# Kernel tuning notes

Measured on AMD Instinct MI355X. Metric: run time of the kernel, lower is better.

## Reference

```python
import jax, jax.numpy as jnp
import numpy as np

BS, T, D, H = 1024, 8, 512, 512  # batch, seq_length, input_dim, hidden_dim


def setup_inputs() -> dict:
    key = jax.random.key(0)
    ks = jax.random.split(key, 9)
    s = lambda k, shape, sc=1.0: jax.random.normal(k, shape, dtype=jnp.float32) * sc
    return {
        "x": s(ks[0], (BS, T, D)),
        "h0": s(ks[1], (2, 1, H)),
        "c0": s(ks[2], (2, 1, H)),
        # per-direction LSTM params; b = b_ih + b_hh combined (identical math)
        "W_ih_f": s(ks[3], (4 * H, D), 0.05),
        "W_hh_f": s(ks[4], (4 * H, H), 0.05),
        "b_f": s(ks[5], (4 * H,), 0.05),
        "W_ih_b": s(ks[6], (4 * H, D), 0.05),
        "W_hh_b": s(ks[7], (4 * H, H), 0.05),
        "b_b": s(ks[8], (4 * H,), 0.05),
    }


def _dir_scan(xg, h0, c0, W_hh):
    """One LSTM direction as a single continuous scan.
    xg: (N, 4H) precomputed input-gate contributions (x @ W_ih.T + b)
    h0, c0: (H,) initial state; W_hh: (4H, H).
    """
    Wt = W_hh.T  # (H, 4H)

    def step(carry, g):
        h, c = carry
        z = g + h @ Wt  # (4H,)
        i, f, gg, o = jnp.split(z, 4)  # PyTorch gate order: i, f, g, o
        i = jax.nn.sigmoid(i)
        f = jax.nn.sigmoid(f)
        gg = jnp.tanh(gg)
        o = jax.nn.sigmoid(o)
        c = f * c + i * gg
        h = o * jnp.tanh(c)
        return (h, c), h

    (hN, cN), hs = jax.lax.scan(step, (h0, c0), xg)
    return hs, hN, cN


def reference(x, h0, c0, W_ih_f, W_hh_f, b_f, W_ih_b, W_hh_b, b_b):
    bs, t, d = x.shape
    hdim = W_hh_f.shape[1]
    # Hidden state is threaded across batch elements in the original loop, so:
    # forward dir == one scan over the flattened (bs*T) sequence,
    # backward dir == one scan over per-sample-reversed then flattened sequence.
    xf = x.reshape(bs * t, d)
    xb = x[:, ::-1, :].reshape(bs * t, d)
    gf = xf @ W_ih_f.T + b_f  # (bs*T, 4H)
    gb = xb @ W_ih_b.T + b_b
    hs_f, hNf, cNf = _dir_scan(gf, h0[0, 0], c0[0, 0], W_hh_f)
    hs_b, hNb, cNb = _dir_scan(gb, h0[1, 0], c0[1, 0], W_hh_b)
    hs_f = hs_f.reshape(bs, t, hdim)
    hs_b = hs_b.reshape(bs, t, hdim)[:, ::-1, :]  # undo per-sample reversal
    out = jnp.concatenate([hs_f, hs_b], axis=-1).reshape(bs * t, 2 * hdim)
    h_n = jnp.stack([hNf, hNb])[:, None, :]  # (2, 1, H)
    c_n = jnp.stack([cNf, cNb])[:, None, :]
    return out, h_n, c_n
```

## Files before the change

kernel.cpp:

```cpp
#include <hip/hip_runtime.h>
#include <stdint.h>

#define BSZ   1024
#define TT    8
#define DD    512
#define HH    512
#define NSEQ  (BSZ*TT)
#define FOURH (4*HH)
#define POISON 0xAAAAAAAAu
#define G_ELEMS  ((size_t)2*NSEQ*FOURH)
#define HB_ELEMS ((size_t)2*(NSEQ+1)*HH)
#define POLL_CAP (1<<16)

typedef __attribute__((ext_vector_type(4))) float vf4;

__device__ __forceinline__ void ld2x16_ic(const float* p, vf4& a, vf4& b){
  asm volatile("global_load_dwordx4 %0, %2, off sc0 sc1\n\t"
               "global_load_dwordx4 %1, %2, off offset:16 sc0 sc1\n\t"
               "s_waitcnt vmcnt(0)"
               : "=v"(a), "=v"(b) : "v"(p) : "memory");
}
__device__ __forceinline__ void st_ic(float* p, float v){
  asm volatile("global_store_dword %0, %1, off sc0 sc1"
               :: "v"(p), "v"(v) : "memory");
}

__global__ void init_hbuf_k(float* __restrict__ hbuf, const float* __restrict__ h0)
{
  size_t idx = (size_t)blockIdx.x*blockDim.x + threadIdx.x;
  if (idx >= HB_ELEMS) return;
  int j = (int)(idx % HH);
  size_t r = idx / HH;
  int t   = (int)(r % (NSEQ+1));
  int dir = (int)(r / (NSEQ+1));
  uint32_t v;
  if (t == 0){
    uint32_t u = __float_as_uint(h0[dir*HH + j]);
    if (u == POISON) u ^= 1u;
    v = u;
  } else {
    v = POISON;
  }
  ((uint32_t*)hbuf)[idx] = v;
}

__global__ __launch_bounds__(256) void gemm_ih_k(
    const float* __restrict__ x,
    const float* __restrict__ Wf, const float* __restrict__ bf,
    const float* __restrict__ Wb, const float* __restrict__ bb,
    float* __restrict__ g)
{
  const int bm = blockIdx.x;
  const int bn = blockIdx.y;
  const int n0  = bm*64;
  const int m0g = bn*64;
  const int dir = m0g >> 11;
  const int m0  = m0g & 2047;
  const float* __restrict__ W    = dir ? Wb : Wf;
  const float* __restrict__ bias = dir ? bb : bf;

  __shared__ float As[32][68];
  __shared__ float Bs[32][68];

  const int tid = threadIdx.x;
  const int tx = tid & 15, ty = tid >> 4;
  float acc[4][4] = {};

  const int lr = tid >> 2;
  const int lk = (tid & 3) * 8;
  int arow = n0 + lr; if (dir) arow ^= 7;
  const float* ap = &x[(size_t)arow*DD];
  const float* wp = &W[(size_t)(m0+lr)*DD];

  for (int k0 = 0; k0 < DD; k0 += 32){
    float4 a0 = *(const float4*)&ap[k0+lk];
    float4 a1 = *(const float4*)&ap[k0+lk+4];
    float4 w0 = *(const float4*)&wp[k0+lk];
    float4 w1 = *(const float4*)&wp[k0+lk+4];
    __syncthreads();
    As[lk+0][lr]=a0.x; As[lk+1][lr]=a0.y; As[lk+2][lr]=a0.z; As[lk+3][lr]=a0.w;
    As[lk+4][lr]=a1.x; As[lk+5][lr]=a1.y; As[lk+6][lr]=a1.z; As[lk+7][lr]=a1.w;
    Bs[lk+0][lr]=w0.x; Bs[lk+1][lr]=w0.y; Bs[lk+2][lr]=w0.z; Bs[lk+3][lr]=w0.w;
    Bs[lk+4][lr]=w1.x; Bs[lk+5][lr]=w1.y; Bs[lk+6][lr]=w1.z; Bs[lk+7][lr]=w1.w;
    __syncthreads();
    #pragma unroll
    for (int kk = 0; kk < 32; kk++){
      float4 av = *(const float4*)&As[kk][ty*4];
      float4 bv = *(const float4*)&Bs[kk][tx*4];
      acc[0][0]+=av.x*bv.x; acc[0][1]+=av.x*bv.y; acc[0][2]+=av.x*bv.z; acc[0][3]+=av.x*bv.w;
      acc[1][0]+=av.y*bv.x; acc[1][1]+=av.y*bv.y; acc[1][2]+=av.y*bv.z; acc[1][3]+=av.y*bv.w;
      acc[2][0]+=av.z*bv.x; acc[2][1]+=av.z*bv.y; acc[2][2]+=av.z*bv.z; acc[2][3]+=av.z*bv.w;
      acc[3][0]+=av.w*bv.x; acc[3][1]+=av.w*bv.y; acc[3][2]+=av.w*bv.z; acc[3][3]+=av.w*bv.w;
    }
  }

  const size_t gbase = (size_t)dir*NSEQ*FOURH;
  #pragma unroll
  for (int i = 0; i < 4; i++){
    const int n = n0 + ty*4 + i;
    #pragma unroll
    for (int j = 0; j < 4; j++){
      const int m = m0 + tx*4 + j;
      g[gbase + (size_t)n*FOURH + m] = acc[i][j] + bias[m];
    }
  }
}

#define DPP_ROR_ADD(v, ctrl) do { \
    int _t = __builtin_amdgcn_update_dpp(0, __float_as_int(v), (ctrl), 0xf, 0xf, false); \
    (v) += __int_as_float(_t); } while (0)

__global__ __launch_bounds__(1024, 4) void scan_k(
    const float* __restrict__ Whh_f, const float* __restrict__ Whh_b,
    const float* __restrict__ c0, const float* __restrict__ g,
    float* __restrict__ hbuf, float* __restrict__ out)
{
  const int bx  = blockIdx.x;
  const int dir = bx >> 5;
  const int w   = bx & 31;
  const int j0  = w << 4;
  const int tid  = threadIdx.x;
  const int lane = tid & 63;
  const int wv   = tid >> 6;
  const int s    = lane & 31;
  const int rb   = lane >> 5;
  const int r0   = (wv << 2) + rb;
  const int r1   = r0 + 2;

  const float* __restrict__ Whh = dir ? Whh_b : Whh_f;

  __shared__ vf4  hsh4[128];
  __shared__ float zbuf[64];
  __shared__ float gsh[64];
  __shared__ int dead;

  float wA[16], wB[16];
  {
    const int gA = r0 >> 4, hA = r0 & 15;
    const int gB = r1 >> 4, hB = r1 & 15;
    const float* pa = &Whh[(size_t)(gA*HH + j0 + hA)*HH + (s<<4)];
    const float* pb = &Whh[(size_t)(gB*HH + j0 + hB)*HH + (s<<4)];
    #pragma unroll
    for (int q = 0; q < 4; q++){
      float4 va = ((const float4*)pa)[q];
      wA[4*q+0]=va.x; wA[4*q+1]=va.y; wA[4*q+2]=va.z; wA[4*q+3]=va.w;
      float4 vb = ((const float4*)pb)[q];
      wB[4*q+0]=vb.x; wB[4*q+1]=vb.y; wB[4*q+2]=vb.z; wB[4*q+3]=vb.w;
    }
  }

  float cst = 0.f;
  if (tid < 16) cst = c0[dir*HH + j0 + tid];
  if (tid == 0) dead = 0;
  __syncthreads();

  float* __restrict__ hb = hbuf + (size_t)dir*(NSEQ+1)*HH;
  const float* __restrict__ gbp = g + (size_t)dir*NSEQ*FOURH;

  const bool gloader = (tid >= 64) && (tid < 80);
  const int  gl = tid - 64;

  for (int t = 0; t < NSEQ; t++){
    float pgi=0.f, pgf=0.f, pgg=0.f, pgo=0.f;
    if (gloader){
      const float* gp = &gbp[(size_t)t*FOURH + j0 + gl];
      pgi = gp[0]; pgf = gp[HH]; pgg = gp[2*HH]; pgo = gp[3*HH];
    }

    if (wv == 0){
      const float* hp = &hb[(size_t)t*HH + (lane<<3)];
      vf4 a, b;
      int it = 0;
      for (;;){
        ld2x16_ic(hp, a, b);
        bool ok = (__float_as_uint(a.x)!=POISON) & (__float_as_uint(a.y)!=POISON)
                & (__float_as_uint(a.z)!=POISON) & (__float_as_uint(a.w)!=POISON)
                & (__float_as_uint(b.x)!=POISON) & (__float_as_uint(b.y)!=POISON)
                & (__float_as_uint(b.z)!=POISON) & (__float_as_uint(b.w)!=POISON);
        if (ok) break;
        if (++it > POLL_CAP){ dead = 1; break; }
        __builtin_amdgcn_s_sleep(1);
      }
      const int c0i = lane << 1;
      const int xo  = (c0i >> 3) & 3;
      hsh4[c0i ^ xo]       = a;
      hsh4[(c0i + 1) ^ xo] = b;
    }
    __syncthreads();
    if (dead) break;

    vf4 h4a, h4b, h4c, h4d;
    {
      const int cb = s << 2;
      h4a = hsh4[(cb+0) ^ (((cb+0)>>3)&3)];
      h4b = hsh4[(cb+1) ^ (((cb+1)>>3)&3)];
      h4c = hsh4[(cb+2) ^ (((cb+2)>>3)&3)];
      h4d = hsh4[(cb+3) ^ (((cb+3)>>3)&3)];
    }

    float a0=0.f, a1=0.f, b0=0.f, b1=0.f;
    a0 += wA[ 0]*h4a.x; a1 += wA[ 1]*h4a.y; a0 += wA[ 2]*h4a.z; a1 += wA[ 3]*h4a.w;
    a0 += wA[ 4]*h4b.x; a1 += wA[ 5]*h4b.y; a0 += wA[ 6]*h4b.z; a1 += wA[ 7]*h4b.w;
    a0 += wA[ 8]*h4c.x; a1 += wA[ 9]*h4c.y; a0 += wA[10]*h4c.z; a1 += wA[11]*h4c.w;
    a0 += wA[12]*h4d.x; a1 += wA[13]*h4d.y; a0 += wA[14]*h4d.z; a1 += wA[15]*h4d.w;
    b0 += wB[ 0]*h4a.x; b1 += wB[ 1]*h4a.y; b0 += wB[ 2]*h4a.z; b1 += wB[ 3]*h4a.w;
    b0 += wB[ 4]*h4b.x; b1 += wB[ 5]*h4b.y; b0 += wB[ 6]*h4b.z; b1 += wB[ 7]*h4b.w;
    b0 += wB[ 8]*h4c.x; b1 += wB[ 9]*h4c.y; b0 += wB[10]*h4c.z; b1 += wB[11]*h4c.w;
    b0 += wB[12]*h4d.x; b1 += wB[13]*h4d.y; b0 += wB[14]*h4d.z; b1 += wB[15]*h4d.w;
    float accA = a0 + a1, accB = b0 + b1;

    DPP_ROR_ADD(accA, 0x128); DPP_ROR_ADD(accA, 0x124);
    DPP_ROR_ADD(accA, 0x122); DPP_ROR_ADD(accA, 0x121);
    accA += __int_as_float(__builtin_amdgcn_ds_swizzle(__float_as_int(accA), 0x401F));
    DPP_ROR_ADD(accB, 0x128); DPP_ROR_ADD(accB, 0x124);
    DPP_ROR_ADD(accB, 0x122); DPP_ROR_ADD(accB, 0x121);
    accB += __int_as_float(__builtin_amdgcn_ds_swizzle(__float_as_int(accB), 0x401F));

    if (s == 0){ zbuf[r0] = accA; zbuf[r1] = accB; }
    if (gloader){ gsh[gl]=pgi; gsh[16+gl]=pgf; gsh[32+gl]=pgg; gsh[48+gl]=pgo; }
    __syncthreads();

    if (tid < 16){
      float zi = zbuf[tid]      + gsh[tid];
      float zf = zbuf[16 + tid] + gsh[16 + tid];
      float zg = zbuf[32 + tid] + gsh[32 + tid];
      float zo = zbuf[48 + tid] + gsh[48 + tid];
      float si = 1.f/(1.f + __expf(-zi));
      float sf = 1.f/(1.f + __expf(-zf));
      float so = 1.f/(1.f + __expf(-zo));
      float e2g = __expf(2.f*zg);
      float tg  = (e2g - 1.f)/(e2g + 1.f);
      cst = sf*cst + si*tg;
      float e2c = __expf(2.f*cst);
      float tc  = (e2c - 1.f)/(e2c + 1.f);
      float hv  = so*tc;
      uint32_t u = __float_as_uint(hv);
      if (u == POISON) hv = __uint_as_float(u ^ 1u);

      const int n = dir ? (t ^ 7) : t;
      out[(size_t)n*(2*HH) + dir*HH + j0 + tid] = hv;

      st_ic(&hb[(size_t)(t+1)*HH + j0 + tid], hv);

      if (t == NSEQ-1){
        out[(size_t)NSEQ*2*HH + dir*HH + j0 + tid] = hv;
        out[(size_t)NSEQ*2*HH + 2*HH + dir*HH + j0 + tid] = cst;
      }
    }
  }
}

extern "C" void kernel_launch(void* const* d_in, const int* in_sizes, int n_in,
                              void* d_out, int out_size, void* d_ws, size_t ws_size,
                              hipStream_t stream)
{
  const float* x    = (const float*)d_in[0];
  const float* h0   = (const float*)d_in[1];
  const float* c0   = (const float*)d_in[2];
  const float* Wihf = (const float*)d_in[3];
  const float* Whhf = (const float*)d_in[4];
  const float* bf   = (const float*)d_in[5];
  const float* Wihb = (const float*)d_in[6];
  const float* Whhb = (const float*)d_in[7];
  const float* bb   = (const float*)d_in[8];
  float* out = (float*)d_out;
  float* ws  = (float*)d_ws;

  float* g    = ws;
  float* hbuf = ws + G_ELEMS;

  {
    int total = (int)HB_ELEMS;
    int blocks = (total + 255) / 256;
    init_hbuf_k<<<blocks, 256, 0, stream>>>(hbuf, h0);
  }
  {
    dim3 grid(NSEQ/64, (2*FOURH)/64);
    gemm_ih_k<<<grid, 256, 0, stream>>>(x, Wihf, bf, Wihb, bb, g);
  }
  scan_k<<<64, 1024, 0, stream>>>(Whhf, Whhb, c0, g, hbuf, out);
}
```

Baseline: 12.70 ms.

## Spread scan blocks across XCDs and poll h via L2 before falling back

Launches 256 blocks and has only two of every eight active, so the working blocks (forward and backward direction pair) end up on the same XCD under round-robin dispatch and share an L2. The h-state polling loop first spins with sc0-only loads, which hit the shared L2, and drops to the old system-coherent sleeping poll only after a bounded number of misses. The h-buffer store is also moved before the out store. This is meant to cut the per-timestep cross-block synchronisation latency. It relies on the block-to-XCD mapping and on L2 coherence among co-located blocks, and the extra idle blocks add a little launch overhead.

Result: slower. 15.28 ms (+20.3%).

```diff
diff --git a/kernel.cpp b/kernel.cpp
--- a/kernel.cpp
+++ b/kernel.cpp
@@ -11,6 +11,7 @@
 #define G_ELEMS  ((size_t)2*NSEQ*FOURH)
 #define HB_ELEMS ((size_t)2*(NSEQ+1)*HH)
 #define POLL_CAP (1<<16)
+#define FAST_CAP 1024
 
 typedef __attribute__((ext_vector_type(4))) float vf4;
 
@@ -20,9 +21,22 @@
                "s_waitcnt vmcnt(0)"
                : "=v"(a), "=v"(b) : "v"(p) : "memory");
 }
+__device__ __forceinline__ void ld2x16_l2(const float* p, vf4& a, vf4& b){
+  asm volatile("global_load_dwordx4 %0, %2, off sc0\n\t"
+               "global_load_dwordx4 %1, %2, off offset:16 sc0\n\t"
+               "s_waitcnt vmcnt(0)"
+               : "=v"(a), "=v"(b) : "v"(p) : "memory");
+}
 __device__ __forceinline__ void st_ic(float* p, float v){
   asm volatile("global_store_dword %0, %1, off sc0 sc1"
                :: "v"(p), "v"(v) : "memory");
+}
+
+__device__ __forceinline__ bool valid8(const vf4& a, const vf4& b){
+  return (__float_as_uint(a.x)!=POISON) & (__float_as_uint(a.y)!=POISON)
+       & (__float_as_uint(a.z)!=POISON) & (__float_as_uint(a.w)!=POISON)
+       & (__float_as_uint(b.x)!=POISON) & (__float_as_uint(b.y)!=POISON)
+       & (__float_as_uint(b.z)!=POISON) & (__float_as_uint(b.w)!=POISON);
 }
 
 __global__ void init_hbuf_k(float* __restrict__ hbuf, const float* __restrict__ h0)
@@ -116,8 +130,10 @@
     float* __restrict__ hbuf, float* __restrict__ out)
 {
   const int bx  = blockIdx.x;
-  const int dir = bx >> 5;
-  const int w   = bx & 31;
+  const int sub = bx & 7;
+  if (sub > 1) return;
+  const int dir = sub;
+  const int w   = bx >> 3;
   const int j0  = w << 4;
   const int tid  = threadIdx.x;
   const int lane = tid & 63;
@@ -160,6 +176,8 @@
   const bool gloader = (tid >= 64) && (tid < 80);
   const int  gl = tid - 64;
 
+  bool slow_lane = false;
+
   for (int t = 0; t < NSEQ; t++){
     float pgi=0.f, pgf=0.f, pgg=0.f, pgo=0.f;
     if (gloader){
@@ -170,16 +188,22 @@
     if (wv == 0){
       const float* hp = &hb[(size_t)t*HH + (lane<<3)];
       vf4 a, b;
-      int it = 0;
-      for (;;){
-        ld2x16_ic(hp, a, b);
-        bool ok = (__float_as_uint(a.x)!=POISON) & (__float_as_uint(a.y)!=POISON)
-                & (__float_as_uint(a.z)!=POISON) & (__float_as_uint(a.w)!=POISON)
-                & (__float_as_uint(b.x)!=POISON) & (__float_as_uint(b.y)!=POISON)
-                & (__float_as_uint(b.z)!=POISON) & (__float_as_uint(b.w)!=POISON);
-        if (ok) break;
-        if (++it > POLL_CAP){ dead = 1; break; }
-        __builtin_amdgcn_s_sleep(1);
+      bool need = true;
+      if (!slow_lane){
+        for (int it = 0; it < FAST_CAP; ++it){
+          ld2x16_l2(hp, a, b);
+          if (valid8(a, b)){ need = false; break; }
+        }
+        if (need) slow_lane = true;
+      }
+      if (need){
+        int it = 0;
+        for (;;){
+          ld2x16_ic(hp, a, b);
+          if (valid8(a, b)) break;
+          if (++it > POLL_CAP){ dead = 1; break; }
+          __builtin_amdgcn_s_sleep(1);
+        }
       }
       const int c0i = lane << 1;
       const int xo  = (c0i >> 3) & 3;
@@ -237,10 +261,10 @@
       uint32_t u = __float_as_uint(hv);
       if (u == POISON) hv = __uint_as_float(u ^ 1u);
 
+      st_ic(&hb[(size_t)(t+1)*HH + j0 + tid], hv);
+
       const int n = dir ? (t ^ 7) : t;
       out[(size_t)n*(2*HH) + dir*HH + j0 + tid] = hv;
-
-      st_ic(&hb[(size_t)(t+1)*HH + j0 + tid], hv);
 
       if (t == NSEQ-1){
         out[(size_t)NSEQ*2*HH + dir*HH + j0 + tid] = hv;
@@ -278,5 +302,5 @@
     dim3 grid(NSEQ/64, (2*FOURH)/64);
     gemm_ih_k<<<grid, 256, 0, stream>>>(x, Wihf, bf, Wihb, bb, g);
   }
-  scan_k<<<64, 1024, 0, stream>>>(Whhf, Whhb, c0, g, hbuf, out);
-}
+  scan_k<<<256, 1024, 0, stream>>>(Whhf, Whhb, c0, g, hbuf, out);
+}
```

## Restructure LSTM scan: one wave per hidden unit, double-buffered h, pipelined polling

Applied to the files above, without the earlier changes.

Work is redistributed so each wave owns one hidden unit and computes all four gates, reduced with DPP and shuffles. This removes the second block barrier and the single 16-thread gate stage. The h vector is double-buffered in shared memory. Polling for the next step's h is issued early as two overlapping in-flight loads, and input-gate values are prefetched one step ahead. The poll cap is lowered, and the code relies on careful waitcnt and sched_barrier ordering, which adds correctness risk in the async polling.

Result: slower. 34.24 ms (+169.7%).

```diff
diff --git a/kernel.cpp b/kernel.cpp
--- a/kernel.cpp
+++ b/kernel.cpp
@@ -10,19 +10,29 @@
 #define POISON 0xAAAAAAAAu
 #define G_ELEMS  ((size_t)2*NSEQ*FOURH)
 #define HB_ELEMS ((size_t)2*(NSEQ+1)*HH)
-#define POLL_CAP (1<<16)
+#define POLL_CAP 4096
 
 typedef __attribute__((ext_vector_type(4))) float vf4;
 
-__device__ __forceinline__ void ld2x16_ic(const float* p, vf4& a, vf4& b){
+__device__ __forceinline__ void poll_issue(const float* p, vf4& a, vf4& b){
   asm volatile("global_load_dwordx4 %0, %2, off sc0 sc1\n\t"
-               "global_load_dwordx4 %1, %2, off offset:16 sc0 sc1\n\t"
-               "s_waitcnt vmcnt(0)"
+               "global_load_dwordx4 %1, %2, off offset:16 sc0 sc1"
                : "=v"(a), "=v"(b) : "v"(p) : "memory");
 }
+#define WAITVM(n)  asm volatile("s_waitcnt vmcnt(" #n ")" ::: "memory")
+#define WAITLGKM() asm volatile("s_waitcnt lgkmcnt(0)" ::: "memory")
+#define SB0()      __builtin_amdgcn_sched_barrier(0)
+
 __device__ __forceinline__ void st_ic(float* p, float v){
   asm volatile("global_store_dword %0, %1, off sc0 sc1"
                :: "v"(p), "v"(v) : "memory");
+}
+
+__device__ __forceinline__ bool valid8(const vf4& a, const vf4& b){
+  return (__float_as_uint(a.x)!=POISON) & (__float_as_uint(a.y)!=POISON)
+       & (__float_as_uint(a.z)!=POISON) & (__float_as_uint(a.w)!=POISON)
+       & (__float_as_uint(b.x)!=POISON) & (__float_as_uint(b.y)!=POISON)
+       & (__float_as_uint(b.z)!=POISON) & (__float_as_uint(b.w)!=POISON);
 }
 
 __global__ void init_hbuf_k(float* __restrict__ hbuf, const float* __restrict__ h0)
@@ -122,130 +132,160 @@
   const int tid  = threadIdx.x;
   const int lane = tid & 63;
   const int wv   = tid >> 6;
-  const int s    = lane & 31;
-  const int rb   = lane >> 5;
-  const int r0   = (wv << 2) + rb;
-  const int r1   = r0 + 2;
+  const int q    = lane >> 4;
+  const int s    = lane & 15;
+  const int sx   = s & 7;
+  const int jmy  = j0 + wv;
 
   const float* __restrict__ Whh = dir ? Whh_b : Whh_f;
 
-  __shared__ vf4  hsh4[128];
-  __shared__ float zbuf[64];
-  __shared__ float gsh[64];
-  __shared__ int dead;
-
-  float wA[16], wB[16];
+  __shared__ vf4  hsh4[2][128];
+  __shared__ float gsh0[4][4];
+  volatile __shared__ int dead;
+
+  float wG[32];
   {
-    const int gA = r0 >> 4, hA = r0 & 15;
-    const int gB = r1 >> 4, hB = r1 & 15;
-    const float* pa = &Whh[(size_t)(gA*HH + j0 + hA)*HH + (s<<4)];
-    const float* pb = &Whh[(size_t)(gB*HH + j0 + hB)*HH + (s<<4)];
+    const float* wp = &Whh[(size_t)(q*HH + jmy)*HH + (s<<5)];
     #pragma unroll
-    for (int q = 0; q < 4; q++){
-      float4 va = ((const float4*)pa)[q];
-      wA[4*q+0]=va.x; wA[4*q+1]=va.y; wA[4*q+2]=va.z; wA[4*q+3]=va.w;
-      float4 vb = ((const float4*)pb)[q];
-      wB[4*q+0]=vb.x; wB[4*q+1]=vb.y; wB[4*q+2]=vb.z; wB[4*q+3]=vb.w;
-    }
-  }
-
-  float cst = 0.f;
-  if (tid < 16) cst = c0[dir*HH + j0 + tid];
+    for (int jj = 0; jj < 8; jj++){
+      float4 v = ((const float4*)wp)[jj];
+      wG[4*jj+0]=v.x; wG[4*jj+1]=v.y; wG[4*jj+2]=v.z; wG[4*jj+3]=v.w;
+    }
+  }
+
+  float cst = c0[dir*HH + jmy];
+
+  float* __restrict__ hb = hbuf + (size_t)dir*(NSEQ+1)*HH;
+  const float* __restrict__ gbp = g + (size_t)dir*NSEQ*FOURH;
+
+  float pg0=0.f, pg1=0.f, pg2=0.f, pg3=0.f;
+  if (wv != 0){
+    const float* gp = &gbp[jmy];
+    pg0 = gp[0]; pg1 = gp[HH]; pg2 = gp[2*HH]; pg3 = gp[3*HH];
+  }
+  if (wv == 1 && lane < 4) gsh0[0][lane] = gbp[lane*HH + j0];
   if (tid == 0) dead = 0;
   __syncthreads();
 
-  float* __restrict__ hb = hbuf + (size_t)dir*(NSEQ+1)*HH;
-  const float* __restrict__ gbp = g + (size_t)dir*NSEQ*FOURH;
-
-  const bool gloader = (tid >= 64) && (tid < 80);
-  const int  gl = tid - 64;
+  vf4 pA0, pB0, pA1, pB1;
+  {
+    const float pz = __uint_as_float(POISON);
+    pA0 = (vf4){pz,pz,pz,pz}; pB0 = pA0; pA1 = pA0; pB1 = pA0;
+  }
+
+  if (wv == 0){
+    const float* hp0 = &hb[(size_t)(lane<<3)];
+    poll_issue(hp0, pA0, pB0);
+    poll_issue(hp0, pA1, pB1);
+  }
 
   for (int t = 0; t < NSEQ; t++){
-    float pgi=0.f, pgf=0.f, pgg=0.f, pgo=0.f;
-    if (gloader){
-      const float* gp = &gbp[(size_t)t*FOURH + j0 + gl];
-      pgi = gp[0]; pgf = gp[HH]; pgg = gp[2*HH]; pgo = gp[3*HH];
-    }
-
     if (wv == 0){
       const float* hp = &hb[(size_t)t*HH + (lane<<3)];
-      vf4 a, b;
-      int it = 0;
-      for (;;){
-        ld2x16_ic(hp, a, b);
-        bool ok = (__float_as_uint(a.x)!=POISON) & (__float_as_uint(a.y)!=POISON)
-                & (__float_as_uint(a.z)!=POISON) & (__float_as_uint(a.w)!=POISON)
-                & (__float_as_uint(b.x)!=POISON) & (__float_as_uint(b.y)!=POISON)
-                & (__float_as_uint(b.z)!=POISON) & (__float_as_uint(b.w)!=POISON);
-        if (ok) break;
-        if (++it > POLL_CAP){ dead = 1; break; }
-        __builtin_amdgcn_s_sleep(1);
+      vf4* dst = &hsh4[t & 1][0];
+      const int c = lane << 1, xo = (c >> 3) & 7;
+      bool got = false;
+      for (int it = 0; it < POLL_CAP && !got; ++it){
+        WAITVM(2); SB0();
+        if (valid8(pA0, pB0)){
+          dst[c ^ xo] = pA0; dst[(c+1) ^ xo] = pB0; got = true;
+        } else {
+          poll_issue(hp, pA0, pB0);
+          WAITVM(2); SB0();
+          if (valid8(pA1, pB1)){
+            dst[c ^ xo] = pA1; dst[(c+1) ^ xo] = pB1; got = true;
+          } else {
+            poll_issue(hp, pA1, pB1);
+          }
+        }
       }
-      const int c0i = lane << 1;
-      const int xo  = (c0i >> 3) & 3;
-      hsh4[c0i ^ xo]       = a;
-      hsh4[(c0i + 1) ^ xo] = b;
-    }
-    __syncthreads();
+      if (!got) dead = 1;
+    }
+    WAITLGKM(); SB0();
+    __builtin_amdgcn_s_barrier(); SB0();
     if (dead) break;
 
-    vf4 h4a, h4b, h4c, h4d;
-    {
-      const int cb = s << 2;
-      h4a = hsh4[(cb+0) ^ (((cb+0)>>3)&3)];
-      h4b = hsh4[(cb+1) ^ (((cb+1)>>3)&3)];
-      h4c = hsh4[(cb+2) ^ (((cb+2)>>3)&3)];
-      h4d = hsh4[(cb+3) ^ (((cb+3)>>3)&3)];
-    }
-
-    float a0=0.f, a1=0.f, b0=0.f, b1=0.f;
-    a0 += wA[ 0]*h4a.x; a1 += wA[ 1]*h4a.y; a0 += wA[ 2]*h4a.z; a1 += wA[ 3]*h4a.w;
-    a0 += wA[ 4]*h4b.x; a1 += wA[ 5]*h4b.y; a0 += wA[ 6]*h4b.z; a1 += wA[ 7]*h4b.w;
-    a0 += wA[ 8]*h4c.x; a1 += wA[ 9]*h4c.y; a0 += wA[10]*h4c.z; a1 += wA[11]*h4c.w;
-    a0 += wA[12]*h4d.x; a1 += wA[13]*h4d.y; a0 += wA[14]*h4d.z; a1 += wA[15]*h4d.w;
-    b0 += wB[ 0]*h4a.x; b1 += wB[ 1]*h4a.y; b0 += wB[ 2]*h4a.z; b1 += wB[ 3]*h4a.w;
-    b0 += wB[ 4]*h4b.x; b1 += wB[ 5]*h4b.y; b0 += wB[ 6]*h4b.z; b1 += wB[ 7]*h4b.w;
-    b0 += wB[ 8]*h4c.x; b1 += wB[ 9]*h4c.y; b0 += wB[10]*h4c.z; b1 += wB[11]*h4c.w;
-    b0 += wB[12]*h4d.x; b1 += wB[13]*h4d.y; b0 += wB[14]*h4d.z; b1 += wB[15]*h4d.w;
-    float accA = a0 + a1, accB = b0 + b1;
-
-    DPP_ROR_ADD(accA, 0x128); DPP_ROR_ADD(accA, 0x124);
-    DPP_ROR_ADD(accA, 0x122); DPP_ROR_ADD(accA, 0x121);
-    accA += __int_as_float(__builtin_amdgcn_ds_swizzle(__float_as_int(accA), 0x401F));
-    DPP_ROR_ADD(accB, 0x128); DPP_ROR_ADD(accB, 0x124);
-    DPP_ROR_ADD(accB, 0x122); DPP_ROR_ADD(accB, 0x121);
-    accB += __int_as_float(__builtin_amdgcn_ds_swizzle(__float_as_int(accB), 0x401F));
-
-    if (s == 0){ zbuf[r0] = accA; zbuf[r1] = accB; }
-    if (gloader){ gsh[gl]=pgi; gsh[16+gl]=pgf; gsh[32+gl]=pgg; gsh[48+gl]=pgo; }
-    __syncthreads();
-
-    if (tid < 16){
-      float zi = zbuf[tid]      + gsh[tid];
-      float zf = zbuf[16 + tid] + gsh[16 + tid];
-      float zg = zbuf[32 + tid] + gsh[32 + tid];
-      float zo = zbuf[48 + tid] + gsh[48 + tid];
-      float si = 1.f/(1.f + __expf(-zi));
-      float sf = 1.f/(1.f + __expf(-zf));
-      float so = 1.f/(1.f + __expf(-zo));
-      float e2g = __expf(2.f*zg);
-      float tg  = (e2g - 1.f)/(e2g + 1.f);
-      cst = sf*cst + si*tg;
-      float e2c = __expf(2.f*cst);
-      float tc  = (e2c - 1.f)/(e2c + 1.f);
-      float hv  = so*tc;
-      uint32_t u = __float_as_uint(hv);
-      if (u == POISON) hv = __uint_as_float(u ^ 1u);
-
+    float ng0=0.f, ng1=0.f, ng2=0.f, ng3=0.f;
+    float n00=0.f, n01=0.f, n02=0.f, n03=0.f;
+    if (wv >= 1 && t+1 < NSEQ){
+      const float* gp = &gbp[(size_t)(t+1)*FOURH + ((wv==1) ? j0 : jmy)];
+      if (wv == 1){
+        n00 = gp[0]; n01 = gp[HH]; n02 = gp[2*HH]; n03 = gp[3*HH];
+        ng0 = gp[1]; ng1 = gp[HH+1]; ng2 = gp[2*HH+1]; ng3 = gp[3*HH+1];
+      } else {
+        ng0 = gp[0]; ng1 = gp[HH]; ng2 = gp[2*HH]; ng3 = gp[3*HH];
+      }
+    }
+
+    const vf4* hv4 = hsh4[t & 1];
+    const int cb = s << 3;
+    vf4 h0_ = hv4[cb + (0 ^ sx)];
+    vf4 h1_ = hv4[cb + (1 ^ sx)];
+    vf4 h2_ = hv4[cb + (2 ^ sx)];
+    vf4 h3_ = hv4[cb + (3 ^ sx)];
+    vf4 h4_ = hv4[cb + (4 ^ sx)];
+    vf4 h5_ = hv4[cb + (5 ^ sx)];
+    vf4 h6_ = hv4[cb + (6 ^ sx)];
+    vf4 h7_ = hv4[cb + (7 ^ sx)];
+
+    float a0=0.f, a1=0.f, a2=0.f, a3=0.f;
+    a0+=wG[ 0]*h0_.x; a1+=wG[ 1]*h0_.y; a2+=wG[ 2]*h0_.z; a3+=wG[ 3]*h0_.w;
+    a0+=wG[ 4]*h1_.x; a1+=wG[ 5]*h1_.y; a2+=wG[ 6]*h1_.z; a3+=wG[ 7]*h1_.w;
+    a0+=wG[ 8]*h2_.x; a1+=wG[ 9]*h2_.y; a2+=wG[10]*h2_.z; a3+=wG[11]*h2_.w;
+    a0+=wG[12]*h3_.x; a1+=wG[13]*h3_.y; a2+=wG[14]*h3_.z; a3+=wG[15]*h3_.w;
+    a0+=wG[16]*h4_.x; a1+=wG[17]*h4_.y; a2+=wG[18]*h4_.z; a3+=wG[19]*h4_.w;
+    a0+=wG[20]*h5_.x; a1+=wG[21]*h5_.y; a2+=wG[22]*h5_.z; a3+=wG[23]*h5_.w;
+    a0+=wG[24]*h6_.x; a1+=wG[25]*h6_.y; a2+=wG[26]*h6_.z; a3+=wG[27]*h6_.w;
+    a0+=wG[28]*h7_.x; a1+=wG[29]*h7_.y; a2+=wG[30]*h7_.z; a3+=wG[31]*h7_.w;
+    float zacc = (a0 + a2) + (a1 + a3);
+
+    DPP_ROR_ADD(zacc, 0x128); DPP_ROR_ADD(zacc, 0x124);
+    DPP_ROR_ADD(zacc, 0x122); DPP_ROR_ADD(zacc, 0x121);
+
+    float zi = __shfl(zacc, 0);
+    float zf = __shfl(zacc, 16);
+    float zg = __shfl(zacc, 32);
+    float zo = __shfl(zacc, 48);
+
+    float gi, gf, gg, go;
+    if (wv == 0){ gi = gsh0[t&3][0]; gf = gsh0[t&3][1];
+                  gg = gsh0[t&3][2]; go = gsh0[t&3][3]; }
+    else        { gi = pg0; gf = pg1; gg = pg2; go = pg3; }
+
+    zi += gi; zf += gf; zg += gg; zo += go;
+    float si = 1.f/(1.f + __expf(-zi));
+    float sf = 1.f/(1.f + __expf(-zf));
+    float so = 1.f/(1.f + __expf(-zo));
+    float e2g = __expf(2.f*zg);
+    float tg  = (e2g - 1.f)/(e2g + 1.f);
+    cst = sf*cst + si*tg;
+    float e2c = __expf(2.f*cst);
+    float tc  = (e2c - 1.f)/(e2c + 1.f);
+    float hv  = so*tc;
+    uint32_t u = __float_as_uint(hv);
+    if (u == POISON) hv = __uint_as_float(u ^ 1u);
+
+    if (lane == 0){
+      st_ic(&hb[(size_t)(t+1)*HH + jmy], hv);
       const int n = dir ? (t ^ 7) : t;
-      out[(size_t)n*(2*HH) + dir*HH + j0 + tid] = hv;
-
-      st_ic(&hb[(size_t)(t+1)*HH + j0 + tid], hv);
-
+      out[(size_t)n*(2*HH) + dir*HH + jmy] = hv;
       if (t == NSEQ-1){
-        out[(size_t)NSEQ*2*HH + dir*HH + j0 + tid] = hv;
-        out[(size_t)NSEQ*2*HH + 2*HH + dir*HH + j0 + tid] = cst;
+        out[(size_t)NSEQ*2*HH + dir*HH + jmy] = hv;
+        out[(size_t)NSEQ*2*HH + 2*HH + dir*HH + jmy] = cst;
       }
+    }
+
+    if (wv == 1 && t+1 < NSEQ && lane < 4){
+      gsh0[(t+1)&3][lane] = (lane==0) ? n00 : (lane==1) ? n01
+                          : (lane==2) ? n02 : n03;
+    }
+    if (wv >= 1){ pg0 = ng0; pg1 = ng1; pg2 = ng2; pg3 = ng3; }
+
+    if (wv == 0 && t < NSEQ-1){
+      const float* hpn = &hb[(size_t)(t+1)*HH + (lane<<3)];
+      poll_issue(hpn, pA0, pB0);
+      __builtin_amdgcn_s_sleep(4);
+      poll_issue(hpn, pA1, pB1);
     }
   }
 }
```

## Pipeline h-state polling with double-buffered in-flight loads and raw barriers

Applied to the files above, without the earlier changes.

Replaces the blocking poll loop (issue load, wait, check, sleep) with two outstanding load pairs that are issued right after the h store and checked alternately, so polling latency overlaps with the other blocks' progress. __syncthreads is replaced with explicit lgkmcnt waits plus s_barrier, and scheduling barriers are added. The W_hh register layout becomes interleaved so the LDS swizzle can be removed. Gate math switches to hardware rcp, which lowers precision slightly. The asm loads sit outside the compiler's dependency tracking, so correctness depends on the manual vmcnt waits being right.

New measurement: 14.23 ms. 1.12x slower.

```diff
diff --git a/kernel.cpp b/kernel.cpp
--- a/kernel.cpp
+++ b/kernel.cpp
@@ -10,19 +10,29 @@
 #define POISON 0xAAAAAAAAu
 #define G_ELEMS  ((size_t)2*NSEQ*FOURH)
 #define HB_ELEMS ((size_t)2*(NSEQ+1)*HH)
-#define POLL_CAP (1<<16)
+#define POLL_CAP 16384
 
 typedef __attribute__((ext_vector_type(4))) float vf4;
 
-__device__ __forceinline__ void ld2x16_ic(const float* p, vf4& a, vf4& b){
+__device__ __forceinline__ void poll_issue(const float* p, vf4& a, vf4& b){
   asm volatile("global_load_dwordx4 %0, %2, off sc0 sc1\n\t"
-               "global_load_dwordx4 %1, %2, off offset:16 sc0 sc1\n\t"
-               "s_waitcnt vmcnt(0)"
+               "global_load_dwordx4 %1, %2, off offset:16 sc0 sc1"
                : "=v"(a), "=v"(b) : "v"(p) : "memory");
 }
+#define WAITVM(n)  asm volatile("s_waitcnt vmcnt(" #n ")" ::: "memory")
+#define WAITLGKM() asm volatile("s_waitcnt lgkmcnt(0)" ::: "memory")
+#define SB0()      __builtin_amdgcn_sched_barrier(0)
+
 __device__ __forceinline__ void st_ic(float* p, float v){
   asm volatile("global_store_dword %0, %1, off sc0 sc1"
                :: "v"(p), "v"(v) : "memory");
+}
+
+__device__ __forceinline__ bool valid8(const vf4& a, const vf4& b){
+  return (__float_as_uint(a.x)!=POISON) & (__float_as_uint(a.y)!=POISON)
+       & (__float_as_uint(a.z)!=POISON) & (__float_as_uint(a.w)!=POISON)
+       & (__float_as_uint(b.x)!=POISON) & (__float_as_uint(b.y)!=POISON)
+       & (__float_as_uint(b.z)!=POISON) & (__float_as_uint(b.w)!=POISON);
 }
 
 __global__ void init_hbuf_k(float* __restrict__ hbuf, const float* __restrict__ h0)
@@ -132,19 +142,19 @@
   __shared__ vf4  hsh4[128];
   __shared__ float zbuf[64];
   __shared__ float gsh[64];
-  __shared__ int dead;
+  volatile __shared__ int dead;
 
   float wA[16], wB[16];
   {
     const int gA = r0 >> 4, hA = r0 & 15;
     const int gB = r1 >> 4, hB = r1 & 15;
-    const float* pa = &Whh[(size_t)(gA*HH + j0 + hA)*HH + (s<<4)];
-    const float* pb = &Whh[(size_t)(gB*HH + j0 + hB)*HH + (s<<4)];
+    const float* pa = &Whh[(size_t)(gA*HH + j0 + hA)*HH];
+    const float* pb = &Whh[(size_t)(gB*HH + j0 + hB)*HH];
     #pragma unroll
     for (int q = 0; q < 4; q++){
-      float4 va = ((const float4*)pa)[q];
+      float4 va = *(const float4*)&pa[q*128 + (s<<2)];
       wA[4*q+0]=va.x; wA[4*q+1]=va.y; wA[4*q+2]=va.z; wA[4*q+3]=va.w;
-      float4 vb = ((const float4*)pb)[q];
+      float4 vb = *(const float4*)&pb[q*128 + (s<<2)];
       wB[4*q+0]=vb.x; wB[4*q+1]=vb.y; wB[4*q+2]=vb.z; wB[4*q+3]=vb.w;
     }
   }
@@ -159,6 +169,17 @@
 
   const bool gloader = (tid >= 64) && (tid < 80);
   const int  gl = tid - 64;
+
+  vf4 pA0, pB0, pA1, pB1;
+  {
+    const float pz = __uint_as_float(POISON);
+    pA0 = (vf4){pz,pz,pz,pz}; pB0 = pA0; pA1 = pA0; pB1 = pA0;
+  }
+  if (wv == 0){
+    const float* hp0 = &hb[(size_t)(lane<<3)];
+    poll_issue(hp0, pA0, pB0);
+    poll_issue(hp0, pA1, pB1);
+  }
 
   for (int t = 0; t < NSEQ; t++){
     float pgi=0.f, pgf=0.f, pgg=0.f, pgo=0.f;
@@ -169,34 +190,32 @@
 
     if (wv == 0){
       const float* hp = &hb[(size_t)t*HH + (lane<<3)];
-      vf4 a, b;
-      int it = 0;
-      for (;;){
-        ld2x16_ic(hp, a, b);
-        bool ok = (__float_as_uint(a.x)!=POISON) & (__float_as_uint(a.y)!=POISON)
-                & (__float_as_uint(a.z)!=POISON) & (__float_as_uint(a.w)!=POISON)
-                & (__float_as_uint(b.x)!=POISON) & (__float_as_uint(b.y)!=POISON)
-                & (__float_as_uint(b.z)!=POISON) & (__float_as_uint(b.w)!=POISON);
-        if (ok) break;
-        if (++it > POLL_CAP){ dead = 1; break; }
-        __builtin_amdgcn_s_sleep(1);
+      const int c = lane << 1;
+      bool got = false;
+      for (int it = 0; it < POLL_CAP && !got; ++it){
+        WAITVM(2); SB0();
+        if (valid8(pA0, pB0)){
+          hsh4[c] = pA0; hsh4[c+1] = pB0; got = true;
+        } else {
+          poll_issue(hp, pA0, pB0);
+          WAITVM(2); SB0();
+          if (valid8(pA1, pB1)){
+            hsh4[c] = pA1; hsh4[c+1] = pB1; got = true;
+          } else {
+            poll_issue(hp, pA1, pB1);
+          }
+        }
       }
-      const int c0i = lane << 1;
-      const int xo  = (c0i >> 3) & 3;
-      hsh4[c0i ^ xo]       = a;
-      hsh4[(c0i + 1) ^ xo] = b;
-    }
-    __syncthreads();
+      if (!got) dead = 1;
+    }
+    WAITLGKM(); SB0();
+    __builtin_amdgcn_s_barrier(); SB0();
     if (dead) break;
 
-    vf4 h4a, h4b, h4c, h4d;
-    {
-      const int cb = s << 2;
-      h4a = hsh4[(cb+0) ^ (((cb+0)>>3)&3)];
-      h4b = hsh4[(cb+1) ^ (((cb+1)>>3)&3)];
-      h4c = hsh4[(cb+2) ^ (((cb+2)>>3)&3)];
-      h4d = hsh4[(cb+3) ^ (((cb+3)>>3)&3)];
-    }
+    vf4 h4a = hsh4[s];
+    vf4 h4b = hsh4[32 + s];
+    vf4 h4c = hsh4[64 + s];
+    vf4 h4d = hsh4[96 + s];
 
     float a0=0.f, a1=0.f, b0=0.f, b1=0.f;
     a0 += wA[ 0]*h4a.x; a1 += wA[ 1]*h4a.y; a0 += wA[ 2]*h4a.z; a1 += wA[ 3]*h4a.w;
@@ -218,34 +237,40 @@
 
     if (s == 0){ zbuf[r0] = accA; zbuf[r1] = accB; }
     if (gloader){ gsh[gl]=pgi; gsh[16+gl]=pgf; gsh[32+gl]=pgg; gsh[48+gl]=pgo; }
-    __syncthreads();
+    WAITLGKM(); SB0();
+    __builtin_amdgcn_s_barrier(); SB0();
 
     if (tid < 16){
       float zi = zbuf[tid]      + gsh[tid];
       float zf = zbuf[16 + tid] + gsh[16 + tid];
       float zg = zbuf[32 + tid] + gsh[32 + tid];
       float zo = zbuf[48 + tid] + gsh[48 + tid];
-      float si = 1.f/(1.f + __expf(-zi));
-      float sf = 1.f/(1.f + __expf(-zf));
-      float so = 1.f/(1.f + __expf(-zo));
-      float e2g = __expf(2.f*zg);
-      float tg  = (e2g - 1.f)/(e2g + 1.f);
+      float si = __builtin_amdgcn_rcpf(1.f + __expf(-zi));
+      float sf = __builtin_amdgcn_rcpf(1.f + __expf(-zf));
+      float so = __builtin_amdgcn_rcpf(1.f + __expf(-zo));
+      float tg = 1.f - 2.f*__builtin_amdgcn_rcpf(__expf(2.f*zg) + 1.f);
       cst = sf*cst + si*tg;
-      float e2c = __expf(2.f*cst);
-      float tc  = (e2c - 1.f)/(e2c + 1.f);
+      float tc = 1.f - 2.f*__builtin_amdgcn_rcpf(__expf(2.f*cst) + 1.f);
       float hv  = so*tc;
       uint32_t u = __float_as_uint(hv);
       if (u == POISON) hv = __uint_as_float(u ^ 1u);
 
+      st_ic(&hb[(size_t)(t+1)*HH + j0 + tid], hv);
+
       const int n = dir ? (t ^ 7) : t;
       out[(size_t)n*(2*HH) + dir*HH + j0 + tid] = hv;
-
-      st_ic(&hb[(size_t)(t+1)*HH + j0 + tid], hv);
 
       if (t == NSEQ-1){
         out[(size_t)NSEQ*2*HH + dir*HH + j0 + tid] = hv;
         out[(size_t)NSEQ*2*HH + 2*HH + dir*HH + j0 + tid] = cst;
       }
+    }
+
+    if (wv == 0 && t < NSEQ-1){
+      const float* hpn = &hb[(size_t)(t+1)*HH + (lane<<3)];
+      poll_issue(hpn, pA0, pB0);
+      __builtin_amdgcn_s_sleep(4);
+      poll_issue(hpn, pA1, pB1);
     }
   }
 }
```
